# Performance work log

Measured on AMD Instinct MI355X. Metric: run time of the kernel, lower is better.

The kernel has to match this reference:

```python
import jax, jax.numpy as jnp
import numpy as np

D_MODEL = 1024
NHEAD = 16
HEAD_DIM = D_MODEL // NHEAD
D_FF = 4096
EPS = 1e-5


def _layernorm(x, g, b):
    mu = jnp.mean(x, axis=-1, keepdims=True)
    var = jnp.mean(jnp.square(x - mu), axis=-1, keepdims=True)
    return (x - mu) * jax.lax.rsqrt(var + EPS) * g + b


def setup_inputs() -> dict:
    key = jax.random.key(0)
    ks = jax.random.split(key, 8)

    def xavier(k, shape):
        fan_out, fan_in = shape
        lim = np.sqrt(6.0 / (fan_in + fan_out))
        return jax.random.uniform(k, shape, jnp.float32, -lim, lim)

    x = jax.random.normal(ks[0], (4, 2048, D_MODEL), jnp.float32)
    return {
        "x": x,
        "Wq": xavier(ks[1], (D_MODEL, D_MODEL)), "bq": jnp.zeros((D_MODEL,), jnp.float32),
        "Wk": xavier(ks[2], (D_MODEL, D_MODEL)), "bk": jnp.zeros((D_MODEL,), jnp.float32),
        "Wv": xavier(ks[3], (D_MODEL, D_MODEL)), "bv": jnp.zeros((D_MODEL,), jnp.float32),
        "Wo": xavier(ks[4], (D_MODEL, D_MODEL)), "bo": jnp.zeros((D_MODEL,), jnp.float32),
        "W1": xavier(ks[5], (D_FF, D_MODEL)), "b1": jnp.zeros((D_FF,), jnp.float32),
        "W2": xavier(ks[6], (D_MODEL, D_FF)), "b2": jnp.zeros((D_MODEL,), jnp.float32),
        "ln1_g": jnp.ones((D_MODEL,), jnp.float32), "ln1_b": jnp.zeros((D_MODEL,), jnp.float32),
        "ln2_g": jnp.ones((D_MODEL,), jnp.float32), "ln2_b": jnp.zeros((D_MODEL,), jnp.float32),
    }


def reference(x, Wq, bq, Wk, bk, Wv, bv, Wo, bo, W1, b1, W2, b2, ln1_g, ln1_b, ln2_g, ln2_b):
    B, T, D = x.shape
    H, Hd = NHEAD, HEAD_DIM

    # --- attention sublayer (pre-LN) ---
    residual = x
    xn = _layernorm(x, ln1_g, ln1_b)
    # torch Linear: y = x @ W.T + b
    q = (xn @ Wq.T + bq).reshape(B, T, H, Hd).transpose(0, 2, 1, 3)  # [B,H,T,Hd]
    k = (xn @ Wk.T + bk).reshape(B, T, H, Hd).transpose(0, 2, 1, 3)
    v = (xn @ Wv.T + bv).reshape(B, T, H, Hd).transpose(0, 2, 1, 3)

    scale = Hd ** -0.5
    scores = jnp.einsum('bhqd,bhkd->bhqk', q, k) * scale  # [B,H,T,T]
    attn = jax.nn.softmax(scores, axis=-1)
    out = jnp.einsum('bhqk,bhkd->bhqd', attn, v)           # [B,H,T,Hd]
    out = out.transpose(0, 2, 1, 3).reshape(B, T, D)
    out = out @ Wo.T + bo
    x = residual + out

    # --- FFN sublayer (pre-LN) ---
    residual = x
    xn = _layernorm(x, ln2_g, ln2_b)
    h = jax.nn.relu(xn @ W1.T + b1)
    h = h @ W2.T + b2
    return residual + h
```

## Files before the change

### kernel.cpp

```cpp
#include <hip/hip_runtime.h>
#include <hip/hip_bf16.h>

using bf16 = __hip_bfloat16;
typedef __attribute__((ext_vector_type(8))) short bf16x8;
typedef __attribute__((ext_vector_type(4))) float f32x4;

#define D_MODEL 1024
#define NHEAD 16
#define HEAD_DIM 64
#define D_FF 4096
#define SEQ 2048
#define NTOK 8192

__device__ __forceinline__ void gload16(const void* g, void* l) {
  __builtin_amdgcn_global_load_lds((const __attribute__((address_space(1))) void*)g,
                                   (__attribute__((address_space(3))) void*)l, 16, 0, 0);
}

__device__ __forceinline__ unsigned pkbf16(float lo, float hi) {
  unsigned r;
  asm("v_cvt_pk_bf16_f32 %0, %1, %2" : "=v"(r) : "v"(lo), "v"(hi));
  return r;
}

__device__ __forceinline__ float fexp2(float x) {
  float r;
  asm("v_exp_f32 %0, %1" : "=v"(r) : "v"(x));
  return r;
}

__device__ __forceinline__ float max3f(float a, float b, float c) {
  return fmaxf(fmaxf(a, b), c);
}

__global__ __launch_bounds__(256) void cvt_all(
    const float* __restrict__ W1, const float* __restrict__ W2,
    const float* __restrict__ Wq, const float* __restrict__ Wk,
    const float* __restrict__ Wv, const float* __restrict__ Wo,
    bf16* __restrict__ w1_b, bf16* __restrict__ w2_b,
    bf16* __restrict__ wqkv, bf16* __restrict__ wo_b) {
  const int bid = blockIdx.x;
  const float* src;
  bf16* dst;
  int lb;
  if (bid < 4096) { src = W1; dst = w1_b; lb = bid; }
  else if (bid < 8192) { src = W2; dst = w2_b; lb = bid - 4096; }
  else {
    const int j = (bid - 8192) >> 10;
    lb = (bid - 8192) & 1023;
    if (j == 0) { src = Wq; dst = wqkv; }
    else if (j == 1) { src = Wk; dst = wqkv + 1048576; }
    else if (j == 2) { src = Wv; dst = wqkv + 2097152; }
    else { src = Wo; dst = wo_b; }
  }
  const int i = (lb * 256 + threadIdx.x) * 4;
  const float4 v = *(const float4*)&src[i];
  dst[i + 0] = __float2bfloat16(v.x);
  dst[i + 1] = __float2bfloat16(v.y);
  dst[i + 2] = __float2bfloat16(v.z);
  dst[i + 3] = __float2bfloat16(v.w);
}

__global__ __launch_bounds__(256) void layernorm_kernel(
    const float* __restrict__ xin, const float* __restrict__ g,
    const float* __restrict__ bta, bf16* __restrict__ out) {
  const int row = blockIdx.x, t = threadIdx.x;
  const float4 v = *(const float4*)&xin[(size_t)row * D_MODEL + t * 4];
  float s = v.x + v.y + v.z + v.w;
#pragma unroll
  for (int m = 1; m < 64; m <<= 1) s += __shfl_xor(s, m);
  __shared__ float red[4], red2[4];
  const int w = t >> 6, l = t & 63;
  if (l == 0) red[w] = s;
  __syncthreads();
  const float mu = (red[0] + red[1] + red[2] + red[3]) * (1.f / 1024.f);
  const float d0 = v.x - mu, d1 = v.y - mu, d2 = v.z - mu, d3 = v.w - mu;
  float q = d0 * d0 + d1 * d1 + d2 * d2 + d3 * d3;
#pragma unroll
  for (int m = 1; m < 64; m <<= 1) q += __shfl_xor(q, m);
  if (l == 0) red2[w] = q;
  __syncthreads();
  const float var = (red2[0] + red2[1] + red2[2] + red2[3]) * (1.f / 1024.f);
  const float rs = rsqrtf(var + 1e-5f);
  const float4 gg = *(const float4*)&g[t * 4];
  const float4 bb = *(const float4*)&bta[t * 4];
  bf16* o = out + (size_t)row * D_MODEL + t * 4;
  o[0] = __float2bfloat16(d0 * rs * gg.x + bb.x);
  o[1] = __float2bfloat16(d1 * rs * gg.y + bb.y);
  o[2] = __float2bfloat16(d2 * rs * gg.z + bb.z);
  o[3] = __float2bfloat16(d3 * rs * gg.w + bb.w);
}

template <int MODE>
__global__ __launch_bounds__(512, 2) void gemmA(
    const bf16* __restrict__ A, const bf16* __restrict__ Bw,
    const float* __restrict__ bias0,
    void* __restrict__ out, int M, int N, int K) {
  constexpr int ASZ = 256 * 128;
  constexpr int TILE = ASZ + 256 * 128;
  __shared__ __align__(16) char smem[2 * TILE];

  const int t = threadIdx.x;
  const int l = t & 63, l15 = l & 15, l4 = (l >> 4) & 3;
  const int w = t >> 6, wm = w >> 2, wn = w & 3;
  const int gx = gridDim.x;
  const int nwg = gx * gridDim.y;
  const int bid0 = blockIdx.y * gx + blockIdx.x;
  const int bid = (bid0 & 7) * (nwg >> 3) + (bid0 >> 3);
  const int m0 = (bid / gx) * 256, n0 = (bid % gx) * 256;

  const int sr = t >> 3;
  const int scol = 8 * ((t & 7) ^ (sr & 7));
  const int swz = (l15 & 7) << 4;
  int coff[2];
  coff[0] = (l4 * 16) ^ swz;
  coff[1] = (64 + l4 * 16) ^ swz;

#define ST_A(j, kb, buf)                                          \
  gload16(&A[(size_t)(m0 + (j) * 64 + sr) * K + (kb) + scol],     \
          (void*)(smem + (buf) * TILE + (j) * 8192 + t * 16))
#define ST_B(j, kb, buf)                                          \
  gload16(&Bw[(size_t)(n0 + (j) * 64 + sr) * K + (kb) + scol],    \
          (void*)(smem + (buf) * TILE + ASZ + (j) * 8192 + t * 16))

  f32x4 acc[8][4] = {};
  const int NTm = K >> 6;

  ST_A(0, 0, 0); ST_A(2, 0, 0); ST_B(0, 0, 0); ST_B(1, 0, 0);
  ST_B(2, 0, 0); ST_B(3, 0, 0); ST_A(1, 0, 0); ST_A(3, 0, 0);
  asm volatile("s_waitcnt vmcnt(0)" ::: "memory");
  __builtin_amdgcn_s_barrier();

  for (int kt = 0; kt < NTm; ++kt) {
    const char* cb = smem + (kt & 1) * TILE;
    const int nb = (kt & 1) ^ 1;
    const int kbn = (kt + 1) << 6;
    const bool hasNext = (kt + 1 < NTm);
#pragma unroll
    for (int kk = 0; kk < 2; ++kk) {
      if (hasNext) {
        if (kk == 0) { ST_A(0, kbn, nb); ST_A(2, kbn, nb); ST_B(0, kbn, nb); ST_B(1, kbn, nb); }
        else         { ST_B(2, kbn, nb); ST_B(3, kbn, nb); ST_A(1, kbn, nb); ST_A(3, kbn, nb); }
      }
      bf16x8 af[8], bfr[4];
#pragma unroll
      for (int mf = 0; mf < 8; ++mf)
        af[mf] = *(const bf16x8*)(cb + (wm * 128 + mf * 16 + l15) * 128 + coff[kk]);
#pragma unroll
      for (int nf = 0; nf < 4; ++nf)
        bfr[nf] = *(const bf16x8*)(cb + ASZ + (wn * 64 + nf * 16 + l15) * 128 + coff[kk]);
      __builtin_amdgcn_s_setprio(1);
#pragma unroll
      for (int mf = 0; mf < 8; ++mf)
#pragma unroll
        for (int nf = 0; nf < 4; ++nf)
          acc[mf][nf] = __builtin_amdgcn_mfma_f32_16x16x32_bf16(
              af[mf], bfr[nf], acc[mf][nf], 0, 0, 0);
      __builtin_amdgcn_s_setprio(0);
    }
    asm volatile("s_waitcnt vmcnt(0)" ::: "memory");
    __builtin_amdgcn_s_barrier();
  }
#undef ST_A
#undef ST_B

#pragma unroll
  for (int mf = 0; mf < 8; ++mf) {
#pragma unroll
    for (int nf = 0; nf < 4; ++nf) {
      const int col = n0 + wn * 64 + nf * 16 + l15;
      const float bb = bias0[col];
#pragma unroll
      for (int r = 0; r < 4; ++r) {
        const int row = m0 + wm * 128 + mf * 16 + l4 * 4 + r;
        float y = acc[mf][nf][r] + bb;
        if constexpr (MODE == 1) y = fmaxf(y, 0.f);
        ((bf16*)out)[(size_t)row * N + col] = __float2bfloat16(y);
      }
    }
  }
}

template <int MODE>
__global__ __launch_bounds__(512, 2) void gemmB(
    const bf16* __restrict__ A, const bf16* __restrict__ Bw,
    const float* __restrict__ bias0, const float* __restrict__ bias1,
    const float* __restrict__ bias2, const float* __restrict__ res,
    void* __restrict__ out, int M, int N, int K) {
  constexpr int ASZ = 128 * 128;
  constexpr int TILE = ASZ + 256 * 128;
  __shared__ __align__(16) char smem[3 * TILE];

  const int t = threadIdx.x;
  const int l = t & 63, l15 = l & 15, l4 = (l >> 4) & 3;
  const int w = t >> 6, wm = w >> 2, wn = w & 3;
  const int gx = gridDim.x;
  const int nwg = gx * gridDim.y;
  const int bid0 = blockIdx.y * gx + blockIdx.x;
  const int bid = (bid0 & 7) * (nwg >> 3) + (bid0 >> 3);
  const int m0 = (bid / gx) * 128, n0 = (bid % gx) * 256;

  const int sr = t >> 3;
  const int scol = 8 * ((t & 7) ^ (sr & 7));
  const int swz = (l15 & 7) << 4;
  int coff[2];
  coff[0] = (l4 * 16) ^ swz;
  coff[1] = (64 + l4 * 16) ^ swz;

#define ST_A(j, kb, buf)                                          \
  gload16(&A[(size_t)(m0 + (j) * 64 + sr) * K + (kb) + scol],     \
          (void*)(smem + (buf) * TILE + (j) * 8192 + t * 16))
#define ST_B(j, kb, buf)                                          \
  gload16(&Bw[(size_t)(n0 + (j) * 64 + sr) * K + (kb) + scol],    \
          (void*)(smem + (buf) * TILE + ASZ + (j) * 8192 + t * 16))

  f32x4 acc[4][4] = {};
  const int NTm = K >> 6;

  ST_B(0, 0, 0); ST_B(1, 0, 0); ST_B(2, 0, 0);
  ST_B(3, 0, 0); ST_A(0, 0, 0); ST_A(1, 0, 0);
  ST_B(0, 64, 1); ST_B(1, 64, 1); ST_B(2, 64, 1);
  ST_B(3, 64, 1); ST_A(0, 64, 1); ST_A(1, 64, 1);
  asm volatile("s_waitcnt vmcnt(6)" ::: "memory");
  __builtin_amdgcn_s_barrier();

  for (int kt = 0; kt < NTm; ++kt) {
    const char* cb = smem + (kt % 3) * TILE;
    const int nb = (kt + 2) % 3;
    const int kbn = (kt + 2) << 6;
    const bool iss = (kt + 2 < NTm);
    if (iss) {
      ST_B(0, kbn, nb); ST_B(1, kbn, nb); ST_B(2, kbn, nb);
      ST_B(3, kbn, nb); ST_A(0, kbn, nb); ST_A(1, kbn, nb);
    }
    bf16x8 af[2][4], bfr[2][4];
#pragma unroll
    for (int kk = 0; kk < 2; ++kk) {
#pragma unroll
      for (int mf = 0; mf < 4; ++mf)
        af[kk][mf] = *(const bf16x8*)(cb + (wm * 64 + mf * 16 + l15) * 128 + coff[kk]);
#pragma unroll
      for (int nf = 0; nf < 4; ++nf)
        bfr[kk][nf] = *(const bf16x8*)(cb + ASZ + (wn * 64 + nf * 16 + l15) * 128 + coff[kk]);
    }
    __builtin_amdgcn_s_setprio(1);
#pragma unroll
    for (int kk = 0; kk < 2; ++kk)
#pragma unroll
      for (int mf = 0; mf < 4; ++mf)
#pragma unroll
        for (int nf = 0; nf < 4; ++nf)
          acc[mf][nf] = __builtin_amdgcn_mfma_f32_16x16x32_bf16(
              af[kk][mf], bfr[kk][nf], acc[mf][nf], 0, 0, 0);
    __builtin_amdgcn_s_setprio(0);
    if (iss) asm volatile("s_waitcnt vmcnt(6)" ::: "memory");
    else     asm volatile("s_waitcnt vmcnt(0)" ::: "memory");
    __builtin_amdgcn_s_barrier();
  }
#undef ST_A
#undef ST_B

#pragma unroll
  for (int mf = 0; mf < 4; ++mf) {
#pragma unroll
    for (int nf = 0; nf < 4; ++nf) {
      const int col = n0 + wn * 64 + nf * 16 + l15;
      float bb;
      if constexpr (MODE == 0) {
        const int sel = col >> 10;
        const float* bp = (sel == 0) ? bias0 : ((sel == 1) ? bias1 : bias2);
        bb = bp[col & 1023];
      } else {
        bb = bias0[col];
      }
#pragma unroll
      for (int r = 0; r < 4; ++r) {
        const int row = m0 + wm * 64 + mf * 16 + l4 * 4 + r;
        float y = acc[mf][nf][r] + bb;
        if constexpr (MODE == 0) {
          const int sel = col >> 10;
          const int c10 = col & 1023;
          const size_t dst = (size_t)sel * (NTOK * 1024) +
                             (size_t)((row >> 11) * NHEAD + (c10 >> 6)) * (SEQ * HEAD_DIM) +
                             (size_t)(row & (SEQ - 1)) * HEAD_DIM + (c10 & 63);
          ((bf16*)out)[dst] = __float2bfloat16(y);
        } else {
          y += res[(size_t)row * N + col];
          ((float*)out)[(size_t)row * N + col] = y;
        }
      }
    }
  }
}

#define SCL 0.18033688011112042f
#define NT (SEQ / 64)

__global__ __launch_bounds__(512) void flash_attn(
    const bf16* __restrict__ Q, const bf16* __restrict__ K,
    const bf16* __restrict__ V, bf16* __restrict__ O) {
  __shared__ char smem[32768];
  const int t = threadIdx.x;
  const int w = t >> 6, l = t & 63;
  const int l15 = l & 15, l4 = l >> 4;
  const int bid0 = blockIdx.y * 8 + blockIdx.x;
  const int bid = (bid0 & 7) * 64 + (bid0 >> 3);
  const int bx = bid & 7, bh = bid >> 3;
  const size_t base = (size_t)bh * (SEQ * HEAD_DIM);
  const int q0 = bx * 256 + w * 32;

  int krow[4], kswz[4];
#pragma unroll
  for (int ni = 0; ni < 4; ++ni) {
    const int kr = (ni >> 1) * 32 + (ni & 1) * 4 + (l15 >> 2) * 8 + (l15 & 3);
    krow[ni] = kr * 128;
    kswz[ni] = ((kr & 3) | (((kr >> 3) & 1) << 2)) << 4;
  }

  bf16x8 qf[2][2];
#pragma unroll
  for (int mi = 0; mi < 2; ++mi)
#pragma unroll
    for (int kk = 0; kk < 2; ++kk)
      qf[mi][kk] = *(const bf16x8*)&Q[base + (size_t)(q0 + mi * 16 + l15) * 64 + kk * 32 + l4 * 8];

  bf16x8 ones;
#pragma unroll
  for (int j = 0; j < 8; ++j) ones[j] = (short)0x3F80;

  f32x4 accO[2][4] = {};
  float m_run[2], l_run[2];
#pragma unroll
  for (int mi = 0; mi < 2; ++mi) { m_run[mi] = -1e30f; l_run[mi] = 0.f; }

  short vg[8];

  const int r0 = t >> 3;
  const int c0 = 8 * ((t & 7) ^ ((r0 & 3) | (((r0 >> 3) & 1) << 2)));
  const short* kg = (const short*)K + base + r0 * 64 + c0;
  const int dv = t & 63;
  const int kb8 = (t >> 6) * 8;
  const short* vp = (const short*)V + base + (size_t)kb8 * 64 + dv;
  const int vtbyte = dv * 128 + ((kb8 * 2) ^ ((dv & 7) << 4));

#define STAGE_K(bufofs)                                          \
  {                                                              \
    gload16(kg, (void*)(smem + (bufofs) + w * 1024));            \
    kg += 4096;                                                  \
  }

#define V_GATHER()                                               \
  {                                                              \
    _Pragma("unroll") for (int j_ = 0; j_ < 8; ++j_)             \
        vg[j_] = vp[j_ * 64];                                    \
    vp += 4096;                                                  \
  }

#define VT_WRITE(bufofs)                                         \
  {                                                              \
    bf16x8 vv;                                                   \
    _Pragma("unroll") for (int j_ = 0; j_ < 8; ++j_)             \
        vv[j_] = vg[j_];                                         \
    *(bf16x8*)(smem + (bufofs) + vtbyte) = vv;                   \
  }

  STAGE_K(0);
  V_GATHER();
  VT_WRITE(16384);
  __syncthreads();

  for (int it = 0; it < NT; ++it) {
    const int cur = it & 1;
    const char* Kb = (const char*)smem + cur * 8192;
    const char* Vb = (const char*)smem + 16384 + cur * 8192;
    const bool pre = (it + 1 < NT);
    if (pre) {
      STAGE_K((cur ^ 1) * 8192);
      V_GATHER();
    }

    bf16x8 kf[2][4];
#pragma unroll
    for (int kk = 0; kk < 2; ++kk)
#pragma unroll
      for (int ni = 0; ni < 4; ++ni)
        kf[kk][ni] = *(const bf16x8*)(Kb + krow[ni] + ((kk * 64 + l4 * 16) ^ kswz[ni]));

    unsigned pw[2][8];
#pragma unroll
    for (int mi = 0; mi < 2; ++mi) {
      f32x4 s[4] = {};
      __builtin_amdgcn_s_setprio(1);
#pragma unroll
      for (int kk = 0; kk < 2; ++kk)
#pragma unroll
        for (int ni = 0; ni < 4; ++ni)
          s[ni] = __builtin_amdgcn_mfma_f32_16x16x32_bf16(kf[kk][ni], qf[mi][kk], s[ni], 0, 0, 0);
      __builtin_amdgcn_s_setprio(0);

      const float t0 = max3f(s[0][0], s[0][1], s[0][2]);
      const float t1 = max3f(s[0][3], s[1][0], s[1][1]);
      const float t2 = max3f(s[1][2], s[1][3], s[2][0]);
      const float t3 = max3f(s[2][1], s[2][2], s[2][3]);
      const float t4 = max3f(s[3][0], s[3][1], s[3][2]);
      float mx = fmaxf(max3f(t1, t2, t3), fmaxf(t4, fmaxf(t0, s[3][3])));
      mx = fmaxf(mx, __shfl_xor(mx, 16));
      mx = fmaxf(mx, __shfl_xor(mx, 32));
      const float mxs = mx * SCL;
      if (__any(mxs > m_run[mi] + 8.f)) {
        const float mn = fmaxf(m_run[mi], mxs);
        const float c = fexp2(m_run[mi] - mn);
        m_run[mi] = mn;
        l_run[mi] *= c;
#pragma unroll
        for (int ni = 0; ni < 4; ++ni)
#pragma unroll
          for (int r = 0; r < 4; ++r) accO[mi][ni][r] *= c;
      }
#pragma unroll
      for (int ni = 0; ni < 4; ++ni)
#pragma unroll
        for (int r = 0; r < 4; ++r)
          s[ni][r] = fexp2(fmaf(s[ni][r], SCL, -m_run[mi]));
#pragma unroll
      for (int kk = 0; kk < 2; ++kk)
#pragma unroll
        for (int jj = 0; jj < 4; ++jj) {
          const int ni = 2 * kk + (jj >> 1);
          pw[mi][kk * 4 + jj] = pkbf16(s[ni][2 * (jj & 1)], s[ni][2 * (jj & 1) + 1]);
        }
    }

    f32x4 zz[2] = {};
#pragma unroll
    for (int kk = 0; kk < 2; ++kk) {
      bf16x8 vf[4];
#pragma unroll
      for (int ni = 0; ni < 4; ++ni)
        vf[ni] = *(const bf16x8*)(Vb + (ni * 16 + l15) * 128 +
                                  ((kk * 64 + l4 * 16) ^ ((l15 & 7) << 4)));
#pragma unroll
      for (int mi = 0; mi < 2; ++mi) {
        union { unsigned u[4]; bf16x8 h; } pb;
#pragma unroll
        for (int jj = 0; jj < 4; ++jj) pb.u[jj] = pw[mi][kk * 4 + jj];
        __builtin_amdgcn_s_setprio(1);
#pragma unroll
        for (int ni = 0; ni < 4; ++ni)
          accO[mi][ni] = __builtin_amdgcn_mfma_f32_16x16x32_bf16(vf[ni], pb.h, accO[mi][ni], 0, 0, 0);
        zz[mi] = __builtin_amdgcn_mfma_f32_16x16x32_bf16(ones, pb.h, zz[mi], 0, 0, 0);
        __builtin_amdgcn_s_setprio(0);
      }
    }
#pragma unroll
    for (int mi = 0; mi < 2; ++mi) l_run[mi] += zz[mi][0];

    if (pre) VT_WRITE(16384 + (cur ^ 1) * 8192);
    __syncthreads();
  }

  char* ob = smem + w * 4096;
#pragma unroll
  for (int mi = 0; mi < 2; ++mi) {
    const float inv = 1.f / l_run[mi];
    const int qr = mi * 16 + l15;
    const int sw = (qr & 7) << 4;
#pragma unroll
    for (int ni = 0; ni < 4; ++ni)
#pragma unroll
      for (int rr = 0; rr < 2; ++rr) {
        const unsigned pk = pkbf16(accO[mi][ni][2 * rr] * inv, accO[mi][ni][2 * rr + 1] * inv);
        *(unsigned*)(ob + qr * 128 + ((ni * 32 + l4 * 8 + 4 * rr) ^ sw)) = pk;
      }
  }
  asm volatile("s_waitcnt lgkmcnt(0)" ::: "memory");
  __builtin_amdgcn_sched_barrier(0);

  const int b = bh >> 4, h = bh & 15;
  const int hr = l >> 1, hf = l & 1;
  const size_t orow = ((size_t)b * SEQ + bx * 256 + w * 32 + hr) * D_MODEL + h * HEAD_DIM + hf * 32;
#pragma unroll
  for (int c = 0; c < 4; ++c) {
    bf16x8 vv = *(const bf16x8*)(ob + hr * 128 + (((hf * 64) + c * 16) ^ ((hr & 7) << 4)));
    *(bf16x8*)&O[orow + c * 8] = vv;
  }
}

extern "C" void kernel_launch(void* const* d_in, const int* in_sizes, int n_in,
                              void* d_out, int out_size, void* d_ws, size_t ws_size,
                              hipStream_t stream) {
  const float* x     = (const float*)d_in[0];
  const float* Wq    = (const float*)d_in[1];
  const float* bq    = (const float*)d_in[2];
  const float* Wk    = (const float*)d_in[3];
  const float* bk    = (const float*)d_in[4];
  const float* Wv    = (const float*)d_in[5];
  const float* bv    = (const float*)d_in[6];
  const float* Wo    = (const float*)d_in[7];
  const float* bo    = (const float*)d_in[8];
  const float* W1    = (const float*)d_in[9];
  const float* b1    = (const float*)d_in[10];
  const float* W2    = (const float*)d_in[11];
  const float* b2    = (const float*)d_in[12];
  const float* ln1_g = (const float*)d_in[13];
  const float* ln1_b = (const float*)d_in[14];
  const float* ln2_g = (const float*)d_in[15];
  const float* ln2_b = (const float*)d_in[16];

  const size_t MB = 1ull << 20;
  char* ws = (char*)d_ws;
  bf16* wqkv = (bf16*)(ws + 0 * MB);
  bf16* wo_b = (bf16*)(ws + 6 * MB);
  bf16* w1_b = (bf16*)(ws + 8 * MB);
  bf16* w2_b = (bf16*)(ws + 16 * MB);
  bf16* xn   = (bf16*)(ws + 24 * MB);
  bf16* qb   = (bf16*)(ws + 40 * MB);
  bf16* kbuf = (bf16*)(ws + 56 * MB);
  bf16* vb   = (bf16*)(ws + 72 * MB);
  bf16* hb   = (bf16*)(ws + 40 * MB);
  float* x1  = (float*)(ws + 104 * MB);

  cvt_all<<<12288, 256, 0, stream>>>(W1, W2, Wq, Wk, Wv, Wo, w1_b, w2_b, wqkv, wo_b);

  layernorm_kernel<<<NTOK, 256, 0, stream>>>(x, ln1_g, ln1_b, xn);

  gemmB<0><<<dim3(3072 / 256, NTOK / 128), 512, 0, stream>>>(
      xn, wqkv, bq, bk, bv, nullptr, qb, NTOK, 3072, 1024);

  flash_attn<<<dim3(SEQ / 256, 4 * NHEAD), 512, 0, stream>>>(qb, kbuf, vb, xn);

  gemmB<2><<<dim3(1024 / 256, NTOK / 128), 512, 0, stream>>>(
      xn, wo_b, bo, bo, bo, x, x1, NTOK, 1024, 1024);

  layernorm_kernel<<<NTOK, 256, 0, stream>>>(x1, ln2_g, ln2_b, xn);

  gemmA<1><<<dim3(D_FF / 256, NTOK / 256), 512, 0, stream>>>(
      xn, w1_b, b1, hb, NTOK, D_FF, 1024);

  gemmB<2><<<dim3(1024 / 256, NTOK / 128), 512, 0, stream>>>(
      hb, w2_b, b2, b2, b2, x1, d_out, NTOK, 1024, D_FF);
}
```

Measured before the change: 382.1 us.

## Restructure FFN1 GEMM into four-phase interleaved load/compute pipeline

Replaces the double-buffered 256x256 GEMM used for the FFN up-projection with a schedule that splits each K-tile into four quadrant MFMA phases. Each phase overlaps LDS fragment reads and staggered global-to-LDS loads for the next B tile and the tile after next for A, separated by barriers and explicit waitcnts. The aim is to hide global load latency and LDS read latency behind MFMA work. In exchange it adds more barriers per iteration and a more fragile buffer-reuse ordering, and it remaps accumulator row and column indices in the epilogue.

```diff
diff --git a/kernel.cpp b/kernel.cpp
--- a/kernel.cpp
+++ b/kernel.cpp
@@ -92,13 +92,11 @@
 }
 
 template <int MODE>
-__global__ __launch_bounds__(512, 2) void gemmA(
+__global__ __launch_bounds__(512, 2) void gemm8p(
     const bf16* __restrict__ A, const bf16* __restrict__ Bw,
     const float* __restrict__ bias0,
     void* __restrict__ out, int M, int N, int K) {
-  constexpr int ASZ = 256 * 128;
-  constexpr int TILE = ASZ + 256 * 128;
-  __shared__ __align__(16) char smem[2 * TILE];
+  __shared__ __align__(16) char smem[131072];
 
   const int t = threadIdx.x;
   const int l = t & 63, l15 = l & 15, l4 = (l >> 4) & 3;
@@ -116,63 +114,125 @@
   coff[0] = (l4 * 16) ^ swz;
   coff[1] = (64 + l4 * 16) ^ swz;
 
-#define ST_A(j, kb, buf)                                          \
+#define SA(j, kb, buf)                                            \
   gload16(&A[(size_t)(m0 + (j) * 64 + sr) * K + (kb) + scol],     \
-          (void*)(smem + (buf) * TILE + (j) * 8192 + t * 16))
-#define ST_B(j, kb, buf)                                          \
+          (void*)(smem + (buf) * 65536 + (j) * 8192 + t * 16))
+#define SB(j, kb, buf)                                            \
   gload16(&Bw[(size_t)(n0 + (j) * 64 + sr) * K + (kb) + scol],    \
-          (void*)(smem + (buf) * TILE + ASZ + (j) * 8192 + t * 16))
+          (void*)(smem + (buf) * 65536 + 32768 + (j) * 8192 + t * 16))
 
   f32x4 acc[8][4] = {};
   const int NTm = K >> 6;
 
-  ST_A(0, 0, 0); ST_A(2, 0, 0); ST_B(0, 0, 0); ST_B(1, 0, 0);
-  ST_B(2, 0, 0); ST_B(3, 0, 0); ST_A(1, 0, 0); ST_A(3, 0, 0);
-  asm volatile("s_waitcnt vmcnt(0)" ::: "memory");
+  SA(0, 0, 0); SA(1, 0, 0); SA(2, 0, 0); SA(3, 0, 0);
+  SB(0, 0, 0); SB(1, 0, 0); SB(2, 0, 0); SB(3, 0, 0);
+  SA(0, 64, 1); SA(1, 64, 1); SA(2, 64, 1); SA(3, 64, 1);
+  asm volatile("s_waitcnt vmcnt(4)" ::: "memory");
   __builtin_amdgcn_s_barrier();
 
   for (int kt = 0; kt < NTm; ++kt) {
-    const char* cb = smem + (kt & 1) * TILE;
-    const int nb = (kt & 1) ^ 1;
-    const int kbn = (kt + 1) << 6;
-    const bool hasNext = (kt + 1 < NTm);
+    const char* cb = smem + (kt & 1) * 65536;
+    const int nb1 = (kt & 1) ^ 1;
+    const int nb2 = kt & 1;
+    const int kb1 = (kt + 1) << 6, kb2 = (kt + 2) << 6;
+    const bool s1 = (kt + 1 < NTm), s2 = (kt + 2 < NTm);
+    bf16x8 af0[2][4], af1[2][4], bf0[2][2], bf1[2][2];
+
 #pragma unroll
     for (int kk = 0; kk < 2; ++kk) {
-      if (hasNext) {
-        if (kk == 0) { ST_A(0, kbn, nb); ST_A(2, kbn, nb); ST_B(0, kbn, nb); ST_B(1, kbn, nb); }
-        else         { ST_B(2, kbn, nb); ST_B(3, kbn, nb); ST_A(1, kbn, nb); ST_A(3, kbn, nb); }
-      }
-      bf16x8 af[8], bfr[4];
-#pragma unroll
-      for (int mf = 0; mf < 8; ++mf)
-        af[mf] = *(const bf16x8*)(cb + (wm * 128 + mf * 16 + l15) * 128 + coff[kk]);
-#pragma unroll
-      for (int nf = 0; nf < 4; ++nf)
-        bfr[nf] = *(const bf16x8*)(cb + ASZ + (wn * 64 + nf * 16 + l15) * 128 + coff[kk]);
-      __builtin_amdgcn_s_setprio(1);
-#pragma unroll
-      for (int mf = 0; mf < 8; ++mf)
-#pragma unroll
-        for (int nf = 0; nf < 4; ++nf)
+#pragma unroll
+      for (int mf = 0; mf < 4; ++mf)
+        af0[kk][mf] = *(const bf16x8*)(cb + (wm * 128 + mf * 16 + l15) * 128 + coff[kk]);
+#pragma unroll
+      for (int nf = 0; nf < 2; ++nf)
+        bf0[kk][nf] = *(const bf16x8*)(cb + 32768 + (wn * 64 + nf * 16 + l15) * 128 + coff[kk]);
+    }
+    if (s1) { SB(0, kb1, nb1); SB(1, kb1, nb1); }
+    __builtin_amdgcn_s_barrier();
+    asm volatile("s_waitcnt lgkmcnt(0)" ::: "memory");
+    __builtin_amdgcn_sched_barrier(0);
+    __builtin_amdgcn_s_setprio(1);
+#pragma unroll
+    for (int kk = 0; kk < 2; ++kk)
+#pragma unroll
+      for (int mf = 0; mf < 4; ++mf)
+#pragma unroll
+        for (int nf = 0; nf < 2; ++nf)
           acc[mf][nf] = __builtin_amdgcn_mfma_f32_16x16x32_bf16(
-              af[mf], bfr[nf], acc[mf][nf], 0, 0, 0);
-      __builtin_amdgcn_s_setprio(0);
-    }
-    asm volatile("s_waitcnt vmcnt(0)" ::: "memory");
-    __builtin_amdgcn_s_barrier();
-  }
-#undef ST_A
-#undef ST_B
+              af0[kk][mf], bf0[kk][nf], acc[mf][nf], 0, 0, 0);
+    __builtin_amdgcn_s_setprio(0);
+    __builtin_amdgcn_s_barrier();
+
+#pragma unroll
+    for (int kk = 0; kk < 2; ++kk)
+#pragma unroll
+      for (int mf = 0; mf < 4; ++mf)
+        af1[kk][mf] = *(const bf16x8*)(cb + (wm * 128 + 64 + mf * 16 + l15) * 128 + coff[kk]);
+    if (s1) { SB(2, kb1, nb1); SB(3, kb1, nb1); }
+    __builtin_amdgcn_s_barrier();
+    asm volatile("s_waitcnt lgkmcnt(0)" ::: "memory");
+    __builtin_amdgcn_sched_barrier(0);
+    __builtin_amdgcn_s_setprio(1);
+#pragma unroll
+    for (int kk = 0; kk < 2; ++kk)
+#pragma unroll
+      for (int mf = 0; mf < 4; ++mf)
+#pragma unroll
+        for (int nf = 0; nf < 2; ++nf)
+          acc[4 + mf][nf] = __builtin_amdgcn_mfma_f32_16x16x32_bf16(
+              af1[kk][mf], bf0[kk][nf], acc[4 + mf][nf], 0, 0, 0);
+    __builtin_amdgcn_s_setprio(0);
+    __builtin_amdgcn_s_barrier();
+
+#pragma unroll
+    for (int kk = 0; kk < 2; ++kk)
+#pragma unroll
+      for (int nf = 0; nf < 2; ++nf)
+        bf1[kk][nf] = *(const bf16x8*)(cb + 32768 + (wn * 64 + 32 + nf * 16 + l15) * 128 + coff[kk]);
+    if (s2) { SA(0, kb2, nb2); SA(1, kb2, nb2); }
+    __builtin_amdgcn_s_barrier();
+    asm volatile("s_waitcnt lgkmcnt(0)" ::: "memory");
+    __builtin_amdgcn_sched_barrier(0);
+    __builtin_amdgcn_s_setprio(1);
+#pragma unroll
+    for (int kk = 0; kk < 2; ++kk)
+#pragma unroll
+      for (int mf = 0; mf < 4; ++mf)
+#pragma unroll
+        for (int nf = 0; nf < 2; ++nf)
+          acc[mf][2 + nf] = __builtin_amdgcn_mfma_f32_16x16x32_bf16(
+              af0[kk][mf], bf1[kk][nf], acc[mf][2 + nf], 0, 0, 0);
+    __builtin_amdgcn_s_setprio(0);
+    __builtin_amdgcn_s_barrier();
+
+    if (s2) { SA(2, kb2, nb2); SA(3, kb2, nb2); }
+    __builtin_amdgcn_s_barrier();
+    __builtin_amdgcn_s_setprio(1);
+#pragma unroll
+    for (int kk = 0; kk < 2; ++kk)
+#pragma unroll
+      for (int mf = 0; mf < 4; ++mf)
+#pragma unroll
+        for (int nf = 0; nf < 2; ++nf)
+          acc[4 + mf][2 + nf] = __builtin_amdgcn_mfma_f32_16x16x32_bf16(
+              af1[kk][mf], bf1[kk][nf], acc[4 + mf][2 + nf], 0, 0, 0);
+    __builtin_amdgcn_s_setprio(0);
+    if (s2) asm volatile("s_waitcnt vmcnt(4)" ::: "memory");
+    else    asm volatile("s_waitcnt vmcnt(0)" ::: "memory");
+    __builtin_amdgcn_s_barrier();
+  }
+#undef SA
+#undef SB
 
 #pragma unroll
   for (int mf = 0; mf < 8; ++mf) {
 #pragma unroll
     for (int nf = 0; nf < 4; ++nf) {
-      const int col = n0 + wn * 64 + nf * 16 + l15;
+      const int col = n0 + wn * 64 + ((nf >> 1) * 32) + (nf & 1) * 16 + l15;
       const float bb = bias0[col];
 #pragma unroll
       for (int r = 0; r < 4; ++r) {
-        const int row = m0 + wm * 128 + mf * 16 + l4 * 4 + r;
+        const int row = m0 + wm * 128 + ((mf >> 2) * 64) + (mf & 3) * 16 + l4 * 4 + r;
         float y = acc[mf][nf][r] + bb;
         if constexpr (MODE == 1) y = fmaxf(y, 0.f);
         ((bf16*)out)[(size_t)row * N + col] = __float2bfloat16(y);
@@ -534,7 +594,7 @@
 
   layernorm_kernel<<<NTOK, 256, 0, stream>>>(x1, ln2_g, ln2_b, xn);
 
-  gemmA<1><<<dim3(D_FF / 256, NTOK / 256), 512, 0, stream>>>(
+  gemm8p<1><<<dim3(D_FF / 256, NTOK / 256), 512, 0, stream>>>(
       xn, w1_b, b1, hb, NTOK, D_FF, 1024);
 
   gemmB<2><<<dim3(1024 / 256, NTOK / 128), 512, 0, stream>>>(
```

Result: no change. 384.8 us (+0.7%).

## Fuse weight conversion with first layernorm; compute softmax row sums via shuffles

Applied to the files above, without the earlier changes.

Merges the weight fp32-to-bf16 conversion and the first layernorm into a single launch, so their independent blocks share one grid and a launch is saved. In flash attention, the row-sum of probabilities was computed with an extra MFMA against a ones vector; it is now an in-register sum plus two cross-lane shuffles. The attention kernel also gains a min-blocks-per-CU hint of 4 in its launch bounds, which may limit registers. The shuffle sum adds VALU work in place of matrix-unit work.

```diff
diff --git a/kernel.cpp b/kernel.cpp
--- a/kernel.cpp
+++ b/kernel.cpp
@@ -33,32 +33,62 @@
   return fmaxf(fmaxf(a, b), c);
 }
 
-__global__ __launch_bounds__(256) void cvt_all(
+__global__ __launch_bounds__(256) void cvt_ln(
     const float* __restrict__ W1, const float* __restrict__ W2,
     const float* __restrict__ Wq, const float* __restrict__ Wk,
     const float* __restrict__ Wv, const float* __restrict__ Wo,
     bf16* __restrict__ w1_b, bf16* __restrict__ w2_b,
-    bf16* __restrict__ wqkv, bf16* __restrict__ wo_b) {
+    bf16* __restrict__ wqkv, bf16* __restrict__ wo_b,
+    const float* __restrict__ x, const float* __restrict__ g,
+    const float* __restrict__ bta, bf16* __restrict__ xn) {
   const int bid = blockIdx.x;
-  const float* src;
-  bf16* dst;
-  int lb;
-  if (bid < 4096) { src = W1; dst = w1_b; lb = bid; }
-  else if (bid < 8192) { src = W2; dst = w2_b; lb = bid - 4096; }
-  else {
-    const int j = (bid - 8192) >> 10;
-    lb = (bid - 8192) & 1023;
-    if (j == 0) { src = Wq; dst = wqkv; }
-    else if (j == 1) { src = Wk; dst = wqkv + 1048576; }
-    else if (j == 2) { src = Wv; dst = wqkv + 2097152; }
-    else { src = Wo; dst = wo_b; }
-  }
-  const int i = (lb * 256 + threadIdx.x) * 4;
-  const float4 v = *(const float4*)&src[i];
-  dst[i + 0] = __float2bfloat16(v.x);
-  dst[i + 1] = __float2bfloat16(v.y);
-  dst[i + 2] = __float2bfloat16(v.z);
-  dst[i + 3] = __float2bfloat16(v.w);
+  if (bid < 12288) {
+    const float* src;
+    bf16* dst;
+    int lb;
+    if (bid < 4096) { src = W1; dst = w1_b; lb = bid; }
+    else if (bid < 8192) { src = W2; dst = w2_b; lb = bid - 4096; }
+    else {
+      const int j = (bid - 8192) >> 10;
+      lb = (bid - 8192) & 1023;
+      if (j == 0) { src = Wq; dst = wqkv; }
+      else if (j == 1) { src = Wk; dst = wqkv + 1048576; }
+      else if (j == 2) { src = Wv; dst = wqkv + 2097152; }
+      else { src = Wo; dst = wo_b; }
+    }
+    const int i = (lb * 256 + threadIdx.x) * 4;
+    const float4 v = *(const float4*)&src[i];
+    dst[i + 0] = __float2bfloat16(v.x);
+    dst[i + 1] = __float2bfloat16(v.y);
+    dst[i + 2] = __float2bfloat16(v.z);
+    dst[i + 3] = __float2bfloat16(v.w);
+    return;
+  }
+  const int row = bid - 12288, t = threadIdx.x;
+  const float4 v = *(const float4*)&x[(size_t)row * D_MODEL + t * 4];
+  float s = v.x + v.y + v.z + v.w;
+#pragma unroll
+  for (int m = 1; m < 64; m <<= 1) s += __shfl_xor(s, m);
+  __shared__ float red[4], red2[4];
+  const int w = t >> 6, l = t & 63;
+  if (l == 0) red[w] = s;
+  __syncthreads();
+  const float mu = (red[0] + red[1] + red[2] + red[3]) * (1.f / 1024.f);
+  const float d0 = v.x - mu, d1 = v.y - mu, d2 = v.z - mu, d3 = v.w - mu;
+  float q = d0 * d0 + d1 * d1 + d2 * d2 + d3 * d3;
+#pragma unroll
+  for (int m = 1; m < 64; m <<= 1) q += __shfl_xor(q, m);
+  if (l == 0) red2[w] = q;
+  __syncthreads();
+  const float var = (red2[0] + red2[1] + red2[2] + red2[3]) * (1.f / 1024.f);
+  const float rs = rsqrtf(var + 1e-5f);
+  const float4 gg = *(const float4*)&g[t * 4];
+  const float4 bb = *(const float4*)&bta[t * 4];
+  bf16* o = xn + (size_t)row * D_MODEL + t * 4;
+  o[0] = __float2bfloat16(d0 * rs * gg.x + bb.x);
+  o[1] = __float2bfloat16(d1 * rs * gg.y + bb.y);
+  o[2] = __float2bfloat16(d2 * rs * gg.z + bb.z);
+  o[3] = __float2bfloat16(d3 * rs * gg.w + bb.w);
 }
 
 __global__ __launch_bounds__(256) void layernorm_kernel(
@@ -296,7 +326,7 @@
 #define SCL 0.18033688011112042f
 #define NT (SEQ / 64)
 
-__global__ __launch_bounds__(512) void flash_attn(
+__global__ __launch_bounds__(512, 4) void flash_attn(
     const bf16* __restrict__ Q, const bf16* __restrict__ K,
     const bf16* __restrict__ V, bf16* __restrict__ O) {
   __shared__ char smem[32768];
@@ -323,10 +353,6 @@
 #pragma unroll
     for (int kk = 0; kk < 2; ++kk)
       qf[mi][kk] = *(const bf16x8*)&Q[base + (size_t)(q0 + mi * 16 + l15) * 64 + kk * 32 + l4 * 8];
-
-  bf16x8 ones;
-#pragma unroll
-  for (int j = 0; j < 8; ++j) ones[j] = (short)0x3F80;
 
   f32x4 accO[2][4] = {};
   float m_run[2], l_run[2];
@@ -417,11 +443,18 @@
 #pragma unroll
           for (int r = 0; r < 4; ++r) accO[mi][ni][r] *= c;
       }
+      float rs = 0.f;
 #pragma unroll
       for (int ni = 0; ni < 4; ++ni)
 #pragma unroll
-        for (int r = 0; r < 4; ++r)
-          s[ni][r] = fexp2(fmaf(s[ni][r], SCL, -m_run[mi]));
+        for (int r = 0; r < 4; ++r) {
+          const float p = fexp2(fmaf(s[ni][r], SCL, -m_run[mi]));
+          s[ni][r] = p;
+          rs += p;
+        }
+      rs += __shfl_xor(rs, 16);
+      rs += __shfl_xor(rs, 32);
+      l_run[mi] += rs;
 #pragma unroll
       for (int kk = 0; kk < 2; ++kk)
 #pragma unroll
@@ -431,7 +464,6 @@
         }
     }
 
-    f32x4 zz[2] = {};
 #pragma unroll
     for (int kk = 0; kk < 2; ++kk) {
       bf16x8 vf[4];
@@ -448,12 +480,9 @@
 #pragma unroll
         for (int ni = 0; ni < 4; ++ni)
           accO[mi][ni] = __builtin_amdgcn_mfma_f32_16x16x32_bf16(vf[ni], pb.h, accO[mi][ni], 0, 0, 0);
-        zz[mi] = __builtin_amdgcn_mfma_f32_16x16x32_bf16(ones, pb.h, zz[mi], 0, 0, 0);
         __builtin_amdgcn_s_setprio(0);
       }
     }
-#pragma unroll
-    for (int mi = 0; mi < 2; ++mi) l_run[mi] += zz[mi][0];
 
     if (pre) VT_WRITE(16384 + (cur ^ 1) * 8192);
     __syncthreads();
@@ -520,9 +549,9 @@
   bf16* hb   = (bf16*)(ws + 40 * MB);
   float* x1  = (float*)(ws + 104 * MB);
 
-  cvt_all<<<12288, 256, 0, stream>>>(W1, W2, Wq, Wk, Wv, Wo, w1_b, w2_b, wqkv, wo_b);
-
-  layernorm_kernel<<<NTOK, 256, 0, stream>>>(x, ln1_g, ln1_b, xn);
+  cvt_ln<<<12288 + NTOK, 256, 0, stream>>>(W1, W2, Wq, Wk, Wv, Wo,
+                                           w1_b, w2_b, wqkv, wo_b,
+                                           x, ln1_g, ln1_b, xn);
 
   gemmB<0><<<dim3(3072 / 256, NTOK / 128), 512, 0, stream>>>(
       xn, wqkv, bq, bk, bv, nullptr, qb, NTOK, 3072, 1024);
```

New measurement: 371.8 us. 2.7% less time.
